# Performance work log

Measured on AMD Instinct MI355X. Metric: run time of the kernel, lower is better.

The kernel has to match this reference:

```python
import jax, jax.numpy as jnp
import numpy as np

NEG_SLOPE = 0.2

def _gat_conv(x, src, dst, W, a_src, a_dst, b, heads, out_ch, concat):
    N = x.shape[0]
    h = (x @ W).reshape(N, heads, out_ch)                      # [N,H,C]
    al_s = jnp.einsum('nhc,hc->nh', h, a_src)                  # [N,H]
    al_d = jnp.einsum('nhc,hc->nh', h, a_dst)
    e = jax.nn.leaky_relu(al_s[src] + al_d[dst], NEG_SLOPE)    # [E,H]
    emax = jax.ops.segment_max(e, dst, num_segments=N)         # [N,H]
    ex = jnp.exp(e - emax[dst])
    denom = jax.ops.segment_sum(ex, dst, num_segments=N)
    alpha = ex / denom[dst]                                    # [E,H]
    msg = h[src] * alpha[:, :, None]                           # [E,H,C]
    out = jax.ops.segment_sum(msg, dst, num_segments=N)        # [N,H,C]
    if concat:
        out = out.reshape(N, heads * out_ch)
    else:
        out = out.mean(axis=1)
    return out + b

def _add_self_loops(edge_index, N):
    loops = jnp.arange(N, dtype=edge_index.dtype)
    src = jnp.concatenate([edge_index[0], loops])
    dst = jnp.concatenate([edge_index[1], loops])
    return src, dst

def setup_inputs() -> dict:
    key = jax.random.key(0)
    ks = jax.random.split(key, 16)
    N, E, Fin, C, H, G, OUT = 50000, 1600000, 128, 32, 8, 256, 64
    s = 0.05
    inp = {
        'x': jax.random.normal(ks[0], (N, Fin), jnp.float32),
        'edge_index': jax.random.randint(ks[1], (2, E), 0, N, jnp.int64),
        'batch': jnp.sort(jax.random.randint(ks[2], (N,), 0, G, jnp.int64)),
        'W0': jax.random.normal(ks[3], (Fin, H * C), jnp.float32) * s,
        'a_src0': jax.random.normal(ks[4], (H, C), jnp.float32) * s,
        'a_dst0': jax.random.normal(ks[5], (H, C), jnp.float32) * s,
        'b0': jnp.zeros((H * C,), jnp.float32),
        'W1': jax.random.normal(ks[6], (H * C, H * C), jnp.float32) * s,
        'a_src1': jax.random.normal(ks[7], (H, C), jnp.float32) * s,
        'a_dst1': jax.random.normal(ks[8], (H, C), jnp.float32) * s,
        'b1': jnp.zeros((H * C,), jnp.float32),
        'W2': jax.random.normal(ks[9], (H * C, C), jnp.float32) * s,
        'a_src2': jax.random.normal(ks[10], (1, C), jnp.float32) * s,
        'a_dst2': jax.random.normal(ks[11], (1, C), jnp.float32) * s,
        'b2': jnp.zeros((C,), jnp.float32),
        'lin_w': jax.random.normal(ks[12], (C, OUT), jnp.float32) * s,
        'lin_b': jnp.zeros((OUT,), jnp.float32),
    }
    return inp

def reference(x, edge_index, batch, W0, a_src0, a_dst0, b0, W1, a_src1, a_dst1, b1,
              W2, a_src2, a_dst2, b2, lin_w, lin_b):
    N = x.shape[0]
    G = 256
    src, dst = _add_self_loops(edge_index, N)
    h = jax.nn.relu(_gat_conv(x, src, dst, W0, a_src0, a_dst0, b0, 8, 32, True))
    h = jax.nn.relu(_gat_conv(h, src, dst, W1, a_src1, a_dst1, b1, 8, 32, True))
    h = _gat_conv(h, src, dst, W2, a_src2, a_dst2, b2, 1, 32, True)  # heads=1 concat -> [N,32]
    # global mean pool over graphs
    sums = jax.ops.segment_sum(h, batch, num_segments=G)
    cnts = jax.ops.segment_sum(jnp.ones((N,), h.dtype), batch, num_segments=G)
    pooled = sums / jnp.maximum(cnts, 1.0)[:, None]
    return pooled @ lin_w + lin_b
```

## Files before the change

### kernel.cpp

```cpp
#include <hip/hip_runtime.h>
#include <hip/hip_bf16.h>


#define LRELU(x) ((x) >= 0.f ? (x) : 0.2f * (x))

typedef unsigned short ushort8 __attribute__((ext_vector_type(8)));
typedef __attribute__((ext_vector_type(8))) short bf16x8;
typedef __attribute__((ext_vector_type(4))) float f32x4;

__device__ __forceinline__ float bf2f(unsigned short u) {
    return __uint_as_float(((unsigned)u) << 16);
}
__device__ __forceinline__ unsigned short f2bf(float f) {
    __hip_bfloat16 b = __float2bfloat16(f);
    return *reinterpret_cast<unsigned short*>(&b);
}
__device__ __forceinline__ void gl_lds16(const unsigned short* g, unsigned short* l) {
    __builtin_amdgcn_global_load_lds((const __attribute__((address_space(1))) void*)g,
                                     (__attribute__((address_space(3))) void*)l, 16, 0, 0);
}


__global__ void deg_kernel(const int* __restrict__ dst, int* __restrict__ deg,
                           int E, int N) {
    int i = blockIdx.x * blockDim.x + threadIdx.x;
    if (i < E) atomicAdd(&deg[dst[i]], 1);
    else if (i < E + N) atomicAdd(&deg[i - E], 1);
}

__global__ void scan_kernel(const int* __restrict__ deg, int* __restrict__ rowptr,
                            int n) {
    __shared__ int partial[1024];
    const int tid = threadIdx.x;
    const int chunk = (n + 1023) / 1024;
    const int start = min(tid * chunk, n);
    const int end = min(start + chunk, n);
    int s = 0;
    for (int i = start; i < end; i++) s += deg[i];
    partial[tid] = s;
    __syncthreads();
    for (int o = 1; o < 1024; o <<= 1) {
        int v = (tid >= o) ? partial[tid - o] : 0;
        __syncthreads();
        partial[tid] += v;
        __syncthreads();
    }
    int run = (tid == 0) ? 0 : partial[tid - 1];
    for (int i = start; i < end; i++) { rowptr[i] = run; run += deg[i]; }
    if (tid == 0) rowptr[n] = partial[1023];
}

__global__ void scatter_col_binned(const int* __restrict__ src, const int* __restrict__ dst,
                                   int* __restrict__ rowptr, int* __restrict__ col,
                                   int E, int N, int lo, int hi) {
    int i = blockIdx.x * blockDim.x + threadIdx.x;
    if (i < E) {
        int d = dst[i];
        if (d < lo || d >= hi) return;
        int pos = atomicAdd(&rowptr[d], 1);
        col[pos] = src[i];
    } else if (i < E + N) {
        int d = i - E;
        if (d < lo || d >= hi) return;
        int pos = atomicAdd(&rowptr[d], 1);
        col[pos] = d;
    }
}

__global__ void expand_dst_kernel(const int* __restrict__ rowptr, int* __restrict__ dstA,
                                  int N) {
    int n = blockIdx.x * blockDim.x + threadIdx.x;
    if (n >= N) return;
    int r0 = (n == 0) ? 0 : rowptr[n - 1];
    int r1 = rowptr[n];
    for (int p = r0; p < r1; p++) dstA[p] = n;
}

__global__ void gstart_kernel(const int* __restrict__ batch, int* __restrict__ gstart,
                              int N, int G) {
    int g = blockIdx.x * blockDim.x + threadIdx.x;
    if (g > G) return;
    int lo = 0, hi = N;
    while (lo < hi) { int mid = (lo + hi) >> 1; if (batch[mid] < g) lo = mid + 1; else hi = mid; }
    gstart[g] = lo;
}


__global__ void split_plain_kernel(const float* __restrict__ X, unsigned short* __restrict__ h,
                                   unsigned short* __restrict__ l, int n) {
    int i = blockIdx.x * blockDim.x + threadIdx.x;
    if (i >= n) return;
    float v = X[i];
    unsigned short hb = f2bf(v);
    h[i] = hb;
    l[i] = f2bf(v - bf2f(hb));
}

__global__ void splitT_kernel(const float* __restrict__ W, unsigned short* __restrict__ th,
                              unsigned short* __restrict__ tl, int K, int N) {
    int i = blockIdx.x * blockDim.x + threadIdx.x;
    if (i >= N * K) return;
    int n = i / K, k = i - n * K;
    float v = W[(size_t)k * N + n];
    unsigned short hb = f2bf(v);
    th[i] = hb;
    tl[i] = f2bf(v - bf2f(hb));
}


template <int BM, int BN, int WM, int WN>
__global__ __launch_bounds__(256)
void gemm_mfma_v2(const unsigned short* __restrict__ Ah, const unsigned short* __restrict__ Al,
                  const unsigned short* __restrict__ Bth, const unsigned short* __restrict__ Btl,
                  unsigned short* __restrict__ Cc, int M, int N, int K) {
    constexpr int BK = 32;
    constexpr int MT = WM / 16, NT = WN / 16;
    constexpr int NWX = BN / WN;
    __shared__ __attribute__((aligned(16))) unsigned short Ha[BM][BK];
    __shared__ __attribute__((aligned(16))) unsigned short La[BM][BK];
    __shared__ __attribute__((aligned(16))) unsigned short Hb[BN][BK];
    __shared__ __attribute__((aligned(16))) unsigned short Lb[BN][BK];
    const int tid = threadIdx.x;
    const int lane = tid & 63;
    const int wave = tid >> 6;
    const int wx = wave % NWX, wy = wave / NWX;
    const int by = blockIdx.y * BM;
    const int bx = blockIdx.x * BN;
    const int r16 = lane & 15, kg = lane >> 4;
    const int srow = lane >> 2, sslot = lane & 3;

    f32x4 acc[MT][NT];
#pragma unroll
    for (int i = 0; i < MT; i++)
#pragma unroll
        for (int j = 0; j < NT; j++) acc[i][j] = (f32x4){0.f, 0.f, 0.f, 0.f};

    for (int k0 = 0; k0 < K; k0 += BK) {
        for (int t = wave; t < BM / 16; t += 4) {
            int gm = by + t * 16 + srow;
            if (gm >= M) gm = M - 1;
            const size_t goff = (size_t)gm * K + k0 + sslot * 8;
            gl_lds16(Ah + goff, &Ha[t * 16][0]);
            gl_lds16(Al + goff, &La[t * 16][0]);
        }
        for (int t = wave; t < BN / 16; t += 4) {
            int gn = bx + t * 16 + srow;
            const size_t goff = (size_t)gn * K + k0 + sslot * 8;
            gl_lds16(Bth + goff, &Hb[t * 16][0]);
            gl_lds16(Btl + goff, &Lb[t * 16][0]);
        }
        __syncthreads();
        bf16x8 bh[NT], bl[NT];
#pragma unroll
        for (int j = 0; j < NT; j++) {
            bh[j] = *(const bf16x8*)&Hb[wx * WN + j * 16 + r16][kg * 8];
            bl[j] = *(const bf16x8*)&Lb[wx * WN + j * 16 + r16][kg * 8];
        }
#pragma unroll
        for (int i = 0; i < MT; i++) {
            bf16x8 ah = *(const bf16x8*)&Ha[wy * WM + i * 16 + r16][kg * 8];
            bf16x8 al2 = *(const bf16x8*)&La[wy * WM + i * 16 + r16][kg * 8];
#pragma unroll
            for (int j = 0; j < NT; j++) {
                acc[i][j] = __builtin_amdgcn_mfma_f32_16x16x32_bf16(ah, bh[j], acc[i][j], 0, 0, 0);
                acc[i][j] = __builtin_amdgcn_mfma_f32_16x16x32_bf16(ah, bl[j], acc[i][j], 0, 0, 0);
                acc[i][j] = __builtin_amdgcn_mfma_f32_16x16x32_bf16(al2, bh[j], acc[i][j], 0, 0, 0);
            }
        }
        __syncthreads();
    }
#pragma unroll
    for (int i = 0; i < MT; i++) {
#pragma unroll
        for (int r = 0; r < 4; r++) {
            int gm = by + wy * WM + i * 16 + kg * 4 + r;
            if (gm >= M) continue;
#pragma unroll
            for (int j = 0; j < NT; j++) {
                int gn = bx + wx * WN + j * 16 + r16;
                Cc[(size_t)gm * N + gn] = f2bf(acc[i][j][r]);
            }
        }
    }
}


template <int H, int C>
__global__ void al_bf16(const unsigned short* __restrict__ hfeat, const float* __restrict__ a_src,
                        const float* __restrict__ a_dst, float* __restrict__ als,
                        float* __restrict__ ald, int N) {
    int i = blockIdx.x * blockDim.x + threadIdx.x;
    if (i >= N * H) return;
    int n = i / H, h = i % H;
    const unsigned short* hp = hfeat + (size_t)n * H * C + h * C;
    float s1 = 0.f, s2 = 0.f;
    for (int c0 = 0; c0 < C; c0 += 8) {
        ushort8 v = *(const ushort8*)(hp + c0);
#pragma unroll
        for (int k = 0; k < 8; k++) {
            float f = bf2f(v[k]);
            s1 += f * a_src[h * C + c0 + k];
            s2 += f * a_dst[h * C + c0 + k];
        }
    }
    als[i] = s1;
    ald[i] = s2;
}


__global__ void edge_w_pair(const float* __restrict__ als, const float* __restrict__ ald,
                            const int* __restrict__ col, const int* __restrict__ dstA,
                            unsigned int* __restrict__ wts2, int Etot) {
    int i = blockIdx.x * blockDim.x + threadIdx.x;
    if (i >= Etot * 4) return;
    int pos = i >> 2, hp = i & 3;
    int s = col[pos], d = dstA[pos];
    float2 a = *(const float2*)&als[(size_t)s * 8 + hp * 2];
    float2 b = *(const float2*)&ald[(size_t)d * 8 + hp * 2];
    float e0 = a.x + b.x; e0 = LRELU(e0);
    float e1 = a.y + b.y; e1 = LRELU(e1);
    unsigned lo = f2bf(__expf(e0));
    unsigned hi = f2bf(__expf(e1));
    wts2[i] = lo | (hi << 16);
}

__global__ void edge_w_h1(const float* __restrict__ als, const float* __restrict__ ald,
                          const int* __restrict__ col, const int* __restrict__ dstA,
                          unsigned short* __restrict__ wts, int Etot) {
    int i = blockIdx.x * blockDim.x + threadIdx.x;
    if (i >= Etot) return;
    int s = col[i], d = dstA[i];
    float e = als[s] + ald[d];
    e = LRELU(e);
    wts[i] = f2bf(__expf(e));
}


template <int H, int C, bool RELU, bool SPLIT>
__global__ __launch_bounds__((H * C < 64) ? 64 : H * C)
void gat_agg_v6(const unsigned short* __restrict__ hfeat,
                const unsigned short* __restrict__ wts,
                const int* __restrict__ rowptr,
                const int* __restrict__ col,
                const float* __restrict__ bias, float* __restrict__ outF,
                unsigned short* __restrict__ outH, unsigned short* __restrict__ outL, int N) {
    constexpr int HC = H * C;
    constexpr int BLOCK = (HC < 64) ? 64 : HC;
    constexpr int VEC = 8;
    constexpr int TPE = HC / VEC;
    constexpr int NG = BLOCK / TPE;
    constexpr int NW = BLOCK / 64;
    constexpr int CAP = 128;

    const int n = blockIdx.x;
    const int tid = threadIdx.x;
    const int r0 = (n == 0) ? 0 : rowptr[n - 1];
    const int deg = rowptr[n] - r0;

    __shared__ float se[CAP * H];
    __shared__ float swred[NW * H];
    __shared__ float ssum[H];
    __shared__ float sacc[NG][HC + 4];

    const size_t wbase = (size_t)r0 * H;
    float lsum = 0.f;
    if (deg <= CAP) {
        for (int idx = tid; idx < deg * H; idx += BLOCK) {
            float v = bf2f(wts[wbase + idx]);
            se[idx] = v;
            lsum += v;
        }
    } else {
        for (int idx = tid; idx < deg * H; idx += BLOCK) {
            float v = bf2f(wts[wbase + idx]);
            if (idx < CAP * H) se[idx] = v;
            lsum += v;
        }
    }
#pragma unroll
    for (int off = H; off < 64; off <<= 1) lsum += __shfl_xor(lsum, off);
    if ((tid & 63) < H) swred[(tid >> 6) * H + (tid & (H - 1))] = lsum;
    __syncthreads();
    if (tid < H) {
        float s = 0.f;
#pragma unroll
        for (int ww = 0; ww < NW; ww++) s += swred[ww * H + tid];
        ssum[tid] = s;
    }

    const int g = tid / TPE;
    const int c = tid % TPE;
    const int head = (c * VEC) / C;
    float acc[VEC] = {};
    int j = g;
    if (deg <= CAP) {
        for (; j + 3 * NG < deg; j += 4 * NG) {
            int s0 = col[r0 + j];
            int s1 = col[r0 + j + NG];
            int s2 = col[r0 + j + 2 * NG];
            int s3 = col[r0 + j + 3 * NG];
            float w0 = se[j * H + head];
            float w1 = se[(j + NG) * H + head];
            float w2 = se[(j + 2 * NG) * H + head];
            float w3 = se[(j + 3 * NG) * H + head];
            ushort8 v0 = *(const ushort8*)(hfeat + (size_t)s0 * HC + c * VEC);
            ushort8 v1 = *(const ushort8*)(hfeat + (size_t)s1 * HC + c * VEC);
            ushort8 v2 = *(const ushort8*)(hfeat + (size_t)s2 * HC + c * VEC);
            ushort8 v3 = *(const ushort8*)(hfeat + (size_t)s3 * HC + c * VEC);
#pragma unroll
            for (int k = 0; k < VEC; k++) acc[k] += bf2f(v0[k]) * w0;
#pragma unroll
            for (int k = 0; k < VEC; k++) acc[k] += bf2f(v1[k]) * w1;
#pragma unroll
            for (int k = 0; k < VEC; k++) acc[k] += bf2f(v2[k]) * w2;
#pragma unroll
            for (int k = 0; k < VEC; k++) acc[k] += bf2f(v3[k]) * w3;
        }
        for (; j < deg; j += NG) {
            int s0 = col[r0 + j];
            float w0 = se[j * H + head];
            ushort8 v0 = *(const ushort8*)(hfeat + (size_t)s0 * HC + c * VEC);
#pragma unroll
            for (int k = 0; k < VEC; k++) acc[k] += bf2f(v0[k]) * w0;
        }
    } else {
        for (; j < deg; j += NG) {
            int s0 = col[r0 + j];
            float w0 = bf2f(wts[wbase + (size_t)j * H + head]);
            ushort8 v0 = *(const ushort8*)(hfeat + (size_t)s0 * HC + c * VEC);
#pragma unroll
            for (int k = 0; k < VEC; k++) acc[k] += bf2f(v0[k]) * w0;
        }
    }
    *(float4*)&sacc[g][c * VEC] = (float4){acc[0], acc[1], acc[2], acc[3]};
    *(float4*)&sacc[g][c * VEC + 4] = (float4){acc[4], acc[5], acc[6], acc[7]};
    __syncthreads();

    if (tid < HC) {
        float v = 0.f;
#pragma unroll
        for (int gg = 0; gg < NG; gg++) v += sacc[gg][tid];
        v = v / ssum[tid / C] + bias[tid];
        if (RELU) v = fmaxf(v, 0.f);
        size_t idx = (size_t)n * HC + tid;
        if (SPLIT) {
            unsigned short hb = f2bf(v);
            outH[idx] = hb;
            outL[idx] = f2bf(v - bf2f(hb));
        } else {
            outF[idx] = v;
        }
    }
}


__global__ __launch_bounds__(256)
void pool_final_kernel(const float* __restrict__ h, const int* __restrict__ gstart,
                       const float* __restrict__ lin_w, const float* __restrict__ lin_b,
                       float* __restrict__ out) {
    const int g = blockIdx.x;
    const int tid = threadIdx.x;
    const int n0 = gstart[g], n1 = gstart[g + 1];
    const int r = tid >> 5, c = tid & 31;
    __shared__ float pp[4][32];
    __shared__ float pm[32];
    float acc = 0.f;
    for (int n = n0 + r; n < n1; n += 8) acc += h[(size_t)n * 32 + c];
    acc += __shfl_xor(acc, 32);
    if ((tid & 63) < 32) pp[tid >> 6][c] = acc;
    __syncthreads();
    if (tid < 32) {
        float s = pp[0][tid] + pp[1][tid] + pp[2][tid] + pp[3][tid];
        pm[tid] = s / fmaxf((float)(n1 - n0), 1.f);
    }
    __syncthreads();
    if (tid < 64) {
        float a = lin_b[tid];
#pragma unroll 8
        for (int cc = 0; cc < 32; cc++) a += pm[cc] * lin_w[cc * 64 + tid];
        out[(size_t)g * 64 + tid] = a;
    }
}


extern "C" void kernel_launch(void* const* d_in, const int* in_sizes, int n_in,
                              void* d_out, int out_size, void* d_ws, size_t ws_size,
                              hipStream_t stream) {
    const float* x     = (const float*)d_in[0];
    const int*   ei    = (const int*)d_in[1];
    const int*   batch = (const int*)d_in[2];
    const float* W0    = (const float*)d_in[3];
    const float* a_s0  = (const float*)d_in[4];
    const float* a_d0  = (const float*)d_in[5];
    const float* b0    = (const float*)d_in[6];
    const float* W1    = (const float*)d_in[7];
    const float* a_s1  = (const float*)d_in[8];
    const float* a_d1  = (const float*)d_in[9];
    const float* b1    = (const float*)d_in[10];
    const float* W2    = (const float*)d_in[11];
    const float* a_s2  = (const float*)d_in[12];
    const float* a_d2  = (const float*)d_in[13];
    const float* b2    = (const float*)d_in[14];
    const float* lin_w = (const float*)d_in[15];
    const float* lin_b = (const float*)d_in[16];

    const int N = in_sizes[0] / 128;
    const int E = in_sizes[1] / 2;
    const int G = 256;
    const int Etot = E + N;
    const int* src = ei;
    const int* dst = ei + E;

    char* w = (char*)d_ws;
    size_t off = 0;
    auto alloc = [&](size_t bytes) -> void* {
        void* p = (void*)(w + off);
        off += (bytes + 255) & ~(size_t)255;
        return p;
    };
    int* deg    = (int*)alloc((size_t)N * 4);
    int* rowptr = (int*)alloc((size_t)(N + 1) * 4);
    int* colA   = (int*)alloc((size_t)Etot * 4);
    int* dstA   = (int*)alloc((size_t)Etot * 4);
    int* gstart = (int*)alloc((size_t)(G + 1) * 4);
    float* als  = (float*)alloc((size_t)N * 8 * 4);
    float* ald  = (float*)alloc((size_t)N * 8 * 4);
    unsigned short* hb  = (unsigned short*)alloc((size_t)N * 256 * 2);
    unsigned short* wts = (unsigned short*)alloc((size_t)Etot * 8 * 2);
    unsigned short* g0h = (unsigned short*)alloc((size_t)N * 256 * 2);
    unsigned short* g0l = (unsigned short*)alloc((size_t)N * 256 * 2);
    float* out2 = (float*)alloc((size_t)N * 32 * 4);
    unsigned short* w0h = (unsigned short*)alloc((size_t)128 * 256 * 2);
    unsigned short* w0l = (unsigned short*)alloc((size_t)128 * 256 * 2);
    unsigned short* w1h = (unsigned short*)alloc((size_t)256 * 256 * 2);
    unsigned short* w1l = (unsigned short*)alloc((size_t)256 * 256 * 2);
    unsigned short* w2h = (unsigned short*)alloc((size_t)256 * 32 * 2);
    unsigned short* w2l = (unsigned short*)alloc((size_t)256 * 32 * 2);
    unsigned short* xh = g0h;
    unsigned short* xl = g0h + (size_t)N * 128;

    hipMemsetAsync(deg, 0, (size_t)N * 4, stream);

    deg_kernel<<<(Etot + 255) / 256, 256, 0, stream>>>(dst, deg, E, N);
    scan_kernel<<<1, 1024, 0, stream>>>(deg, rowptr, N);
    for (int p = 0; p < 4; p++) {
        int lo = (int)((size_t)N * p / 4);
        int hi = (int)((size_t)N * (p + 1) / 4);
        scatter_col_binned<<<(Etot + 255) / 256, 256, 0, stream>>>(src, dst, rowptr, colA, E, N, lo, hi);
    }
    expand_dst_kernel<<<(N + 255) / 256, 256, 0, stream>>>(rowptr, dstA, N);
    gstart_kernel<<<2, 256, 0, stream>>>(batch, gstart, N, G);

    split_plain_kernel<<<(N * 128 + 255) / 256, 256, 0, stream>>>(x, xh, xl, N * 128);
    splitT_kernel<<<(128 * 256 + 255) / 256, 256, 0, stream>>>(W0, w0h, w0l, 128, 256);
    splitT_kernel<<<(256 * 256 + 255) / 256, 256, 0, stream>>>(W1, w1h, w1l, 256, 256);
    splitT_kernel<<<(256 * 32 + 255) / 256, 256, 0, stream>>>(W2, w2h, w2l, 256, 32);

    const int MB = (N + 127) / 128;

    gemm_mfma_v2<128, 128, 64, 64><<<dim3(2, MB), 256, 0, stream>>>(xh, xl, w0h, w0l, hb, N, 256, 128);
    al_bf16<8, 32><<<(N * 8 + 255) / 256, 256, 0, stream>>>(hb, a_s0, a_d0, als, ald, N);
    edge_w_pair<<<((size_t)Etot * 4 + 255) / 256, 256, 0, stream>>>(als, ald, colA, dstA, (unsigned int*)wts, Etot);
    gat_agg_v6<8, 32, true, true><<<N, 256, 0, stream>>>(hb, wts, rowptr, colA, b0, nullptr, g0h, g0l, N);

    gemm_mfma_v2<128, 128, 64, 64><<<dim3(2, MB), 256, 0, stream>>>(g0h, g0l, w1h, w1l, hb, N, 256, 256);
    al_bf16<8, 32><<<(N * 8 + 255) / 256, 256, 0, stream>>>(hb, a_s1, a_d1, als, ald, N);
    edge_w_pair<<<((size_t)Etot * 4 + 255) / 256, 256, 0, stream>>>(als, ald, colA, dstA, (unsigned int*)wts, Etot);
    gat_agg_v6<8, 32, true, true><<<N, 256, 0, stream>>>(hb, wts, rowptr, colA, b1, nullptr, g0h, g0l, N);

    gemm_mfma_v2<128, 32, 32, 32><<<dim3(1, MB), 256, 0, stream>>>(g0h, g0l, w2h, w2l, hb, N, 32, 256);
    al_bf16<1, 32><<<(N + 255) / 256, 256, 0, stream>>>(hb, a_s2, a_d2, als, ald, N);
    edge_w_h1<<<(Etot + 255) / 256, 256, 0, stream>>>(als, ald, colA, dstA, wts, Etot);
    gat_agg_v6<1, 32, false, false><<<N, 64, 0, stream>>>(hb, wts, rowptr, colA, b2, out2, nullptr, nullptr, N);

    pool_final_kernel<<<G, 256, 0, stream>>>(out2, gstart, lin_w, lin_b, (float*)d_out);
}
```

Measured before the change: 708.7 us.

## Aggregate 8-head GAT layers with one wavefront per node instead of a block

Replaces the block-per-node aggregation for the 8-head layers with a wavefront-per-node kernel (4 nodes per block). Each lane owns 4 contiguous channels, so every edge gives one coalesced 512-byte row load, and neighbor indices are staged in LDS and broadcast via readfirstlane. Weight sums use vectorized loads and wave shuffles, which removes the block syncs and the cross-group LDS reduction. The single-head layer gets a specialized kernel with a simpler sum reduction. The cost is serial per-edge iteration within a wave, which gives less memory-level parallelism per node than the old 32-group scheme.

```diff
diff --git a/kernel.cpp b/kernel.cpp
--- a/kernel.cpp
+++ b/kernel.cpp
@@ -5,6 +5,7 @@
 #define LRELU(x) ((x) >= 0.f ? (x) : 0.2f * (x))
 
 typedef unsigned short ushort8 __attribute__((ext_vector_type(8)));
+typedef unsigned short ushort4v __attribute__((ext_vector_type(4)));
 typedef __attribute__((ext_vector_type(8))) short bf16x8;
 typedef __attribute__((ext_vector_type(4))) float f32x4;
 
@@ -236,101 +237,154 @@
 }
 
 
-template <int H, int C, bool RELU, bool SPLIT>
-__global__ __launch_bounds__((H * C < 64) ? 64 : H * C)
-void gat_agg_v6(const unsigned short* __restrict__ hfeat,
+__global__ __launch_bounds__(256)
+void gat_agg_w8(const unsigned short* __restrict__ hfeat,
                 const unsigned short* __restrict__ wts,
                 const int* __restrict__ rowptr,
                 const int* __restrict__ col,
-                const float* __restrict__ bias, float* __restrict__ outF,
-                unsigned short* __restrict__ outH, unsigned short* __restrict__ outL, int N) {
-    constexpr int HC = H * C;
-    constexpr int BLOCK = (HC < 64) ? 64 : HC;
-    constexpr int VEC = 8;
-    constexpr int TPE = HC / VEC;
-    constexpr int NG = BLOCK / TPE;
-    constexpr int NW = BLOCK / 64;
+                const float* __restrict__ bias,
+                unsigned short* __restrict__ outH, unsigned short* __restrict__ outL,
+                int N) {
     constexpr int CAP = 128;
-
+    const int wid = threadIdx.x >> 6;
+    const int lane = threadIdx.x & 63;
+    const int n = blockIdx.x * 4 + wid;
+    __shared__ float se_all[4][CAP * 8];
+    __shared__ int scol_all[4][CAP];
+    if (n >= N) return;
+    float* se = se_all[wid];
+    int* scol = scol_all[wid];
+
+    const int r0 = (n == 0) ? 0 : rowptr[n - 1];
+    const int deg = rowptr[n] - r0;
+    const int dh8 = deg * 8;
+    const size_t wbase = (size_t)r0 * 8;
+    const int dcap = min(deg, CAP);
+
+    for (int j = lane; j < dcap; j += 64) scol[j] = col[r0 + j];
+
+    float p0 = 0.f, p1 = 0.f, p2 = 0.f, p3 = 0.f, p4 = 0.f, p5 = 0.f, p6 = 0.f, p7 = 0.f;
+    for (int base = 0; base < dh8; base += 512) {
+        int idx = base + lane * 8;
+        if (idx < dh8) {
+            ushort8 v = *(const ushort8*)&wts[wbase + idx];
+            float f0 = bf2f(v[0]), f1 = bf2f(v[1]), f2 = bf2f(v[2]), f3 = bf2f(v[3]);
+            float f4 = bf2f(v[4]), f5 = bf2f(v[5]), f6 = bf2f(v[6]), f7 = bf2f(v[7]);
+            p0 += f0; p1 += f1; p2 += f2; p3 += f3;
+            p4 += f4; p5 += f5; p6 += f6; p7 += f7;
+            if (idx < CAP * 8) {
+                *(float4*)&se[idx] = (float4){f0, f1, f2, f3};
+                *(float4*)&se[idx + 4] = (float4){f4, f5, f6, f7};
+            }
+        }
+    }
+#pragma unroll
+    for (int m = 1; m < 64; m <<= 1) {
+        p0 += __shfl_xor(p0, m); p1 += __shfl_xor(p1, m);
+        p2 += __shfl_xor(p2, m); p3 += __shfl_xor(p3, m);
+        p4 += __shfl_xor(p4, m); p5 += __shfl_xor(p5, m);
+        p6 += __shfl_xor(p6, m); p7 += __shfl_xor(p7, m);
+    }
+    const int q = lane >> 3;
+    float S = (q == 0) ? p0 : (q == 1) ? p1 : (q == 2) ? p2 : (q == 3) ? p3
+            : (q == 4) ? p4 : (q == 5) ? p5 : (q == 6) ? p6 : p7;
+    const float sinv = 1.0f / S;
+
+    const int cb = lane * 4;
+    float a0 = 0.f, a1 = 0.f, a2 = 0.f, a3 = 0.f;
+    int j = 0;
+    for (; j + 3 < dcap; j += 4) {
+        int s0 = __builtin_amdgcn_readfirstlane(scol[j]);
+        int s1 = __builtin_amdgcn_readfirstlane(scol[j + 1]);
+        int s2 = __builtin_amdgcn_readfirstlane(scol[j + 2]);
+        int s3 = __builtin_amdgcn_readfirstlane(scol[j + 3]);
+        ushort4v v0 = *(const ushort4v*)(hfeat + (size_t)s0 * 256 + cb);
+        ushort4v v1 = *(const ushort4v*)(hfeat + (size_t)s1 * 256 + cb);
+        ushort4v v2 = *(const ushort4v*)(hfeat + (size_t)s2 * 256 + cb);
+        ushort4v v3 = *(const ushort4v*)(hfeat + (size_t)s3 * 256 + cb);
+        float w0 = se[j * 8 + q];
+        float w1 = se[j * 8 + 8 + q];
+        float w2 = se[j * 8 + 16 + q];
+        float w3 = se[j * 8 + 24 + q];
+        a0 += bf2f(v0[0]) * w0; a1 += bf2f(v0[1]) * w0; a2 += bf2f(v0[2]) * w0; a3 += bf2f(v0[3]) * w0;
+        a0 += bf2f(v1[0]) * w1; a1 += bf2f(v1[1]) * w1; a2 += bf2f(v1[2]) * w1; a3 += bf2f(v1[3]) * w1;
+        a0 += bf2f(v2[0]) * w2; a1 += bf2f(v2[1]) * w2; a2 += bf2f(v2[2]) * w2; a3 += bf2f(v2[3]) * w2;
+        a0 += bf2f(v3[0]) * w3; a1 += bf2f(v3[1]) * w3; a2 += bf2f(v3[2]) * w3; a3 += bf2f(v3[3]) * w3;
+    }
+    for (; j < dcap; j++) {
+        int s0 = __builtin_amdgcn_readfirstlane(scol[j]);
+        ushort4v v0 = *(const ushort4v*)(hfeat + (size_t)s0 * 256 + cb);
+        float w0 = se[j * 8 + q];
+        a0 += bf2f(v0[0]) * w0; a1 += bf2f(v0[1]) * w0; a2 += bf2f(v0[2]) * w0; a3 += bf2f(v0[3]) * w0;
+    }
+    for (; j < deg; j++) {
+        int s0 = col[r0 + j];
+        float w0 = bf2f(wts[wbase + (size_t)j * 8 + q]);
+        ushort4v v0 = *(const ushort4v*)(hfeat + (size_t)s0 * 256 + cb);
+        a0 += bf2f(v0[0]) * w0; a1 += bf2f(v0[1]) * w0; a2 += bf2f(v0[2]) * w0; a3 += bf2f(v0[3]) * w0;
+    }
+
+    float4 b4 = *(const float4*)&bias[cb];
+    float o0 = fmaxf(a0 * sinv + b4.x, 0.f);
+    float o1 = fmaxf(a1 * sinv + b4.y, 0.f);
+    float o2 = fmaxf(a2 * sinv + b4.z, 0.f);
+    float o3 = fmaxf(a3 * sinv + b4.w, 0.f);
+    unsigned short h0 = f2bf(o0), h1 = f2bf(o1), h2 = f2bf(o2), h3 = f2bf(o3);
+    const size_t ob = (size_t)n * 256 + cb;
+    *(ushort4v*)&outH[ob] = (ushort4v){h0, h1, h2, h3};
+    *(ushort4v*)&outL[ob] = (ushort4v){f2bf(o0 - bf2f(h0)), f2bf(o1 - bf2f(h1)),
+                                       f2bf(o2 - bf2f(h2)), f2bf(o3 - bf2f(h3))};
+}
+
+
+__global__ __launch_bounds__(64)
+void gat_agg_h1(const unsigned short* __restrict__ hfeat,
+                const unsigned short* __restrict__ wts,
+                const int* __restrict__ rowptr, const int* __restrict__ col,
+                const float* __restrict__ bias, float* __restrict__ out, int N) {
+    constexpr int HC = 32, VEC = 8, TPE = 4, NG = 16, CAP = 128;
     const int n = blockIdx.x;
     const int tid = threadIdx.x;
     const int r0 = (n == 0) ? 0 : rowptr[n - 1];
     const int deg = rowptr[n] - r0;
 
-    __shared__ float se[CAP * H];
-    __shared__ float swred[NW * H];
-    __shared__ float ssum[H];
+    __shared__ float se[CAP];
     __shared__ float sacc[NG][HC + 4];
-
-    const size_t wbase = (size_t)r0 * H;
+    __shared__ float ssum_s;
+
+    const size_t wbase = (size_t)r0;
     float lsum = 0.f;
-    if (deg <= CAP) {
-        for (int idx = tid; idx < deg * H; idx += BLOCK) {
-            float v = bf2f(wts[wbase + idx]);
-            se[idx] = v;
-            lsum += v;
-        }
-    } else {
-        for (int idx = tid; idx < deg * H; idx += BLOCK) {
-            float v = bf2f(wts[wbase + idx]);
-            if (idx < CAP * H) se[idx] = v;
-            lsum += v;
-        }
-    }
-#pragma unroll
-    for (int off = H; off < 64; off <<= 1) lsum += __shfl_xor(lsum, off);
-    if ((tid & 63) < H) swred[(tid >> 6) * H + (tid & (H - 1))] = lsum;
-    __syncthreads();
-    if (tid < H) {
-        float s = 0.f;
-#pragma unroll
-        for (int ww = 0; ww < NW; ww++) s += swred[ww * H + tid];
-        ssum[tid] = s;
-    }
+    for (int idx = tid; idx < deg; idx += 64) {
+        float v = bf2f(wts[wbase + idx]);
+        if (idx < CAP) se[idx] = v;
+        lsum += v;
+    }
+#pragma unroll
+    for (int off = 1; off < 64; off <<= 1) lsum += __shfl_xor(lsum, off);
+    if (tid == 0) ssum_s = lsum;
 
     const int g = tid / TPE;
     const int c = tid % TPE;
-    const int head = (c * VEC) / C;
     float acc[VEC] = {};
     int j = g;
-    if (deg <= CAP) {
-        for (; j + 3 * NG < deg; j += 4 * NG) {
-            int s0 = col[r0 + j];
-            int s1 = col[r0 + j + NG];
-            int s2 = col[r0 + j + 2 * NG];
-            int s3 = col[r0 + j + 3 * NG];
-            float w0 = se[j * H + head];
-            float w1 = se[(j + NG) * H + head];
-            float w2 = se[(j + 2 * NG) * H + head];
-            float w3 = se[(j + 3 * NG) * H + head];
-            ushort8 v0 = *(const ushort8*)(hfeat + (size_t)s0 * HC + c * VEC);
-            ushort8 v1 = *(const ushort8*)(hfeat + (size_t)s1 * HC + c * VEC);
-            ushort8 v2 = *(const ushort8*)(hfeat + (size_t)s2 * HC + c * VEC);
-            ushort8 v3 = *(const ushort8*)(hfeat + (size_t)s3 * HC + c * VEC);
-#pragma unroll
-            for (int k = 0; k < VEC; k++) acc[k] += bf2f(v0[k]) * w0;
-#pragma unroll
-            for (int k = 0; k < VEC; k++) acc[k] += bf2f(v1[k]) * w1;
-#pragma unroll
-            for (int k = 0; k < VEC; k++) acc[k] += bf2f(v2[k]) * w2;
-#pragma unroll
-            for (int k = 0; k < VEC; k++) acc[k] += bf2f(v3[k]) * w3;
-        }
-        for (; j < deg; j += NG) {
-            int s0 = col[r0 + j];
-            float w0 = se[j * H + head];
-            ushort8 v0 = *(const ushort8*)(hfeat + (size_t)s0 * HC + c * VEC);
-#pragma unroll
-            for (int k = 0; k < VEC; k++) acc[k] += bf2f(v0[k]) * w0;
-        }
-    } else {
-        for (; j < deg; j += NG) {
-            int s0 = col[r0 + j];
-            float w0 = bf2f(wts[wbase + (size_t)j * H + head]);
-            ushort8 v0 = *(const ushort8*)(hfeat + (size_t)s0 * HC + c * VEC);
-#pragma unroll
-            for (int k = 0; k < VEC; k++) acc[k] += bf2f(v0[k]) * w0;
-        }
+    for (; j + NG < deg && j + NG <= CAP; j += 2 * NG) {
+        int s0 = col[r0 + j];
+        int s1 = col[r0 + j + NG];
+        float w0 = se[j];
+        float w1 = se[j + NG];
+        ushort8 v0 = *(const ushort8*)(hfeat + (size_t)s0 * HC + c * VEC);
+        ushort8 v1 = *(const ushort8*)(hfeat + (size_t)s1 * HC + c * VEC);
+#pragma unroll
+        for (int k = 0; k < VEC; k++) acc[k] += bf2f(v0[k]) * w0;
+#pragma unroll
+        for (int k = 0; k < VEC; k++) acc[k] += bf2f(v1[k]) * w1;
+    }
+    for (; j < deg; j += NG) {
+        int s0 = col[r0 + j];
+        float w0 = (j < CAP) ? se[j] : bf2f(wts[wbase + j]);
+        ushort8 v0 = *(const ushort8*)(hfeat + (size_t)s0 * HC + c * VEC);
+#pragma unroll
+        for (int k = 0; k < VEC; k++) acc[k] += bf2f(v0[k]) * w0;
     }
     *(float4*)&sacc[g][c * VEC] = (float4){acc[0], acc[1], acc[2], acc[3]};
     *(float4*)&sacc[g][c * VEC + 4] = (float4){acc[4], acc[5], acc[6], acc[7]};
@@ -340,16 +394,8 @@
         float v = 0.f;
 #pragma unroll
         for (int gg = 0; gg < NG; gg++) v += sacc[gg][tid];
-        v = v / ssum[tid / C] + bias[tid];
-        if (RELU) v = fmaxf(v, 0.f);
-        size_t idx = (size_t)n * HC + tid;
-        if (SPLIT) {
-            unsigned short hb = f2bf(v);
-            outH[idx] = hb;
-            outL[idx] = f2bf(v - bf2f(hb));
-        } else {
-            outF[idx] = v;
-        }
+        v = v / ssum_s + bias[tid];
+        out[(size_t)n * HC + tid] = v;
     }
 }
 
@@ -461,17 +507,17 @@
     gemm_mfma_v2<128, 128, 64, 64><<<dim3(2, MB), 256, 0, stream>>>(xh, xl, w0h, w0l, hb, N, 256, 128);
     al_bf16<8, 32><<<(N * 8 + 255) / 256, 256, 0, stream>>>(hb, a_s0, a_d0, als, ald, N);
     edge_w_pair<<<((size_t)Etot * 4 + 255) / 256, 256, 0, stream>>>(als, ald, colA, dstA, (unsigned int*)wts, Etot);
-    gat_agg_v6<8, 32, true, true><<<N, 256, 0, stream>>>(hb, wts, rowptr, colA, b0, nullptr, g0h, g0l, N);
+    gat_agg_w8<<<(N + 3) / 4, 256, 0, stream>>>(hb, wts, rowptr, colA, b0, g0h, g0l, N);
 
     gemm_mfma_v2<128, 128, 64, 64><<<dim3(2, MB), 256, 0, stream>>>(g0h, g0l, w1h, w1l, hb, N, 256, 256);
     al_bf16<8, 32><<<(N * 8 + 255) / 256, 256, 0, stream>>>(hb, a_s1, a_d1, als, ald, N);
     edge_w_pair<<<((size_t)Etot * 4 + 255) / 256, 256, 0, stream>>>(als, ald, colA, dstA, (unsigned int*)wts, Etot);
-    gat_agg_v6<8, 32, true, true><<<N, 256, 0, stream>>>(hb, wts, rowptr, colA, b1, nullptr, g0h, g0l, N);
+    gat_agg_w8<<<(N + 3) / 4, 256, 0, stream>>>(hb, wts, rowptr, colA, b1, g0h, g0l, N);
 
     gemm_mfma_v2<128, 32, 32, 32><<<dim3(1, MB), 256, 0, stream>>>(g0h, g0l, w2h, w2l, hb, N, 32, 256);
     al_bf16<1, 32><<<(N + 255) / 256, 256, 0, stream>>>(hb, a_s2, a_d2, als, ald, N);
     edge_w_h1<<<(Etot + 255) / 256, 256, 0, stream>>>(als, ald, colA, dstA, wts, Etot);
-    gat_agg_v6<1, 32, false, false><<<N, 64, 0, stream>>>(hb, wts, rowptr, colA, b2, out2, nullptr, nullptr, N);
+    gat_agg_h1<<<N, 64, 0, stream>>>(hb, wts, rowptr, colA, b2, out2, N);
 
     pool_final_kernel<<<G, 256, 0, stream>>>(out2, gstart, lin_w, lin_b, (float*)d_out);
 }
```

New measurement: 678.7 us. -4.2%, faster.
